# Performance work log

Hardware: AMD Instinct MI355X
Metric: run time of the kernel (lower is better)

The kernel has to match this reference:

```python
import jax, jax.numpy as jnp
import numpy as np

B, C, T = 8, 512, 1024
H = 8
D = C // H          # head_dim = 64
K = 64              # max_rel_dist
REL = 2 * K + 1     # 129


def setup_inputs() -> dict:
    key = jax.random.key(0)
    ks = jax.random.split(key, 12)
    s = 0.02
    return {
        "x": jax.random.normal(ks[0], (B, C, T), jnp.float32),
        "x_mask": jnp.ones((B, 1, T), jnp.float32),
        "W_q": jax.random.normal(ks[1], (C, C), jnp.float32) * s,
        "b_q": jnp.zeros((C,), jnp.float32),
        "W_k": jax.random.normal(ks[2], (C, C), jnp.float32) * s,
        "b_k": jnp.zeros((C,), jnp.float32),
        "W_v": jax.random.normal(ks[3], (C, C), jnp.float32) * s,
        "b_v": jnp.zeros((C,), jnp.float32),
        "W_o": jax.random.normal(ks[4], (C, C), jnp.float32) * s,
        "b_o": jnp.zeros((C,), jnp.float32),
        "emb_rel_k": jax.random.normal(ks[5], (REL, D), jnp.float32) * 0.01,
        "emb_rel_v": jax.random.normal(ks[6], (REL, D), jnp.float32) * 0.01,
    }


def _conv1x1(x, W, b):
    # Conv1d with kernel_size=1: (B,C,T) x (Cout,Cin) -> (B,Cout,T)
    return jnp.einsum("oc,bct->bot", W, x) + b[None, :, None]


def _shape_heads(x):
    # (B,C,T) -> (B,H,T,D)
    b = x.shape[0]
    return x.reshape(b, H, D, T).transpose(0, 1, 3, 2)


def reference(x, x_mask, W_q, b_q, W_k, b_k, W_v, b_v, W_o, b_o, emb_rel_k, emb_rel_v):
    q = _shape_heads(_conv1x1(x, W_q, b_q))  # (B,H,T,D)
    k = _shape_heads(_conv1x1(x, W_k, b_k))
    v = _shape_heads(_conv1x1(x, W_v, b_v))

    # relative position indices: clamp(j - i, -K, K) + K  -> (T,T)
    pos = jnp.arange(T)
    rel_idx = jnp.clip(pos[None, :] - pos[:, None], -K, K) + K

    # scores: scaled QK^T plus unscaled relative-key term (faithful to source)
    attn = jnp.einsum("bhid,bhjd->bhij", q, k) / (D ** 0.5)
    rel_k_tt = emb_rel_k[rel_idx]            # (T,T,D)
    attn = attn + jnp.einsum("bhid,ijd->bhij", q, rel_k_tt)

    # key mask: positions with x_mask <= 0 get -1e9
    key_mask = (x_mask <= 0).reshape(x.shape[0], 1, 1, T)
    attn = jnp.where(key_mask, -1e9, attn)
    attn = jax.nn.softmax(attn, axis=-1)     # dropout p=0.0 -> identity

    y = jnp.einsum("bhij,bhjd->bhid", attn, v)
    rel_v_tt = emb_rel_v[rel_idx]            # (T,T,D)
    y = y + jnp.einsum("bhij,ijd->bhid", attn, rel_v_tt)

    # (B,H,T,D) -> (B,H,D,T) -> (B,C,T)
    y = y.transpose(0, 1, 3, 2).reshape(x.shape[0], C, T)
    y = _conv1x1(y, W_o, b_o)
    return y * x_mask
```

## Files before the change

kernel.cpp:

```cpp
#include <hip/hip_runtime.h>

#define B_   8
#define C_   512
#define T_   1024
#define H_   8
#define D_   64
#define K_   64
#define REL_ 129

typedef unsigned short u16;
typedef __attribute__((ext_vector_type(8))) short short8;
typedef __attribute__((ext_vector_type(4))) float f32x4;

__device__ __forceinline__ float b2f(u16 u) {
    return __uint_as_float(((unsigned)u) << 16);
}
__device__ __forceinline__ u16 f2b(float f) {
    unsigned x = __float_as_uint(f);
    x += 0x7fffu + ((x >> 16) & 1u);
    return (u16)(x >> 16);
}

__global__ __launch_bounds__(256) void cast_all_kernel(
    const float* __restrict__ x,
    const float* __restrict__ Wq, const float* __restrict__ Wk,
    const float* __restrict__ Wv, const float* __restrict__ Wo,
    const float* __restrict__ erk, const float* __restrict__ erv,
    u16* __restrict__ xt, u16* __restrict__ Wh,
    u16* __restrict__ ervt, u16* __restrict__ erkb)
{
    __shared__ u16 tile[64][72];
    const int blk = blockIdx.x;
    const int tid = threadIdx.x;
    if (blk < 1024) {
        const int t0 = (blk & 15) * 64, c0 = ((blk >> 4) & 7) * 64, b = blk >> 7;
        const int f = tid & 15, r0 = tid >> 4;
#pragma unroll
        for (int p = 0; p < 4; ++p) {
            const int c = r0 + p * 16;
            const float4 v = *(const float4*)(x + ((size_t)b * C_ + c0 + c) * T_ + t0 + f * 4);
            tile[c][f * 4 + 0] = f2b(v.x);
            tile[c][f * 4 + 1] = f2b(v.y);
            tile[c][f * 4 + 2] = f2b(v.z);
            tile[c][f * 4 + 3] = f2b(v.w);
        }
        __syncthreads();
#pragma unroll
        for (int p = 0; p < 4; ++p) {
            const int t = r0 + p * 16;
            ushort4 u;
            u.x = tile[f * 4 + 0][t];
            u.y = tile[f * 4 + 1][t];
            u.z = tile[f * 4 + 2][t];
            u.w = tile[f * 4 + 3][t];
            *(ushort4*)(xt + ((size_t)b * T_ + t0 + t) * C_ + c0 + f * 4) = u;
        }
    } else if (blk < 2048) {
        const int gid = (blk - 1024) * 256 + tid;
        const int s = gid >> 16;
        const int off = (gid & 65535) * 4;
        const float* W = (s == 0) ? Wq : (s == 1) ? Wk : (s == 2) ? Wv : Wo;
        const float4 v = *(const float4*)(W + off);
        ushort4 u;
        u.x = f2b(v.x); u.y = f2b(v.y); u.z = f2b(v.z); u.w = f2b(v.w);
        *(ushort4*)(Wh + ((size_t)s << 18) + off) = u;
    } else {
        const int idx = (blk - 2048) * 256 + tid;
        if (idx < 64 * 160) {
            const int d = idx / 160, rel = idx % 160;
            ervt[idx] = (rel < REL_) ? f2b(erv[rel * D_ + d]) : (u16)0;
        } else {
            const int j = idx - 64 * 160;
            if (j < REL_ * D_) erkb[j] = f2b(erk[j]);
        }
    }
}

__global__ __launch_bounds__(256) void proj_mfma(
    const u16* __restrict__ xt, const u16* __restrict__ Wh,
    const float* __restrict__ bq, const float* __restrict__ bk, const float* __restrict__ bv,
    u16* __restrict__ qh, u16* __restrict__ kh, u16* __restrict__ vt)
{
    __shared__ u16 Wt[64][72];

    const int t0 = blockIdx.x * 64;
    const int h  = blockIdx.y;
    const int sel = blockIdx.z >> 3;
    const int b   = blockIdx.z & 7;
    const int tid = threadIdx.x, wave = tid >> 6, lane = tid & 63;
    const int quad = lane >> 4, l16 = lane & 15;

    const u16* Wbase = Wh + ((size_t)sel << 18) + ((size_t)(h * 64) << 9);
    const u16* A = xt + (((size_t)b * T_ + t0 + wave * 16 + l16) << 9);

    const int so = tid >> 2;
    const int sc = (tid & 3) * 16;
    const u16* wsrc = Wbase + ((size_t)so << 9) + sc;

    f32x4 acc[4] = {{0.f,0.f,0.f,0.f},{0.f,0.f,0.f,0.f},{0.f,0.f,0.f,0.f},{0.f,0.f,0.f,0.f}};

    uint4 wv0 = *(const uint4*)(wsrc);
    uint4 wv1 = *(const uint4*)(wsrc + 8);
#pragma unroll 1
    for (int i = 0; i < 8; ++i) {
        const int c0 = i * 64;
        __syncthreads();
        *(uint4*)&Wt[so][sc] = wv0;
        *(uint4*)&Wt[so][sc + 8] = wv1;
        __syncthreads();
        if (i < 7) {
            wv0 = *(const uint4*)(wsrc + c0 + 64);
            wv1 = *(const uint4*)(wsrc + c0 + 72);
        }
#pragma unroll
        for (int kk = 0; kk < 64; kk += 32) {
            const short8 af = *(const short8*)(A + c0 + kk + quad * 8);
#pragma unroll
            for (int nt = 0; nt < 4; ++nt) {
                const short8 bf = *(const short8*)(&Wt[nt * 16 + l16][kk + quad * 8]);
                acc[nt] = __builtin_amdgcn_mfma_f32_16x16x32_bf16(af, bf, acc[nt], 0, 0, 0);
            }
        }
    }

    const float* bias = (sel == 0) ? bq : (sel == 1) ? bk : bv;
    const int bh = b * 8 + h;
#pragma unroll
    for (int nt = 0; nt < 4; ++nt) {
        const int d = nt * 16 + l16;
        const float bo = bias[h * 64 + d];
#pragma unroll
        for (int rix = 0; rix < 4; ++rix) {
            const int t = t0 + wave * 16 + quad * 4 + rix;
            const u16 val = f2b(acc[nt][rix] + bo);
            if (sel == 2) {
                vt[(((size_t)bh * 64 + d) << 10) + t] = val;
            } else {
                u16* dst = sel ? kh : qh;
                dst[(((size_t)bh * T_ + t) << 6) + d] = val;
            }
        }
    }
}

__global__ __launch_bounds__(256, 2) void attn_kernel(
    const u16* __restrict__ qh, const u16* __restrict__ kh, const u16* __restrict__ vt,
    const u16* __restrict__ erkb, const u16* __restrict__ ervt,
    const float* __restrict__ xmask, u16* __restrict__ yf)
{
    __shared__ u16   Sb[32][1032];
    __shared__ u16   sw[32][168];
    __shared__ float red[4][32][2];
    __shared__ float invrow[32];

    const int gid = blockIdx.x;
    const int x8 = gid & 7, r5 = gid >> 3;
    const int bh = x8 + 8 * (r5 >> 5);
    const int i0 = (r5 & 31) * 32;
    const int b = bh >> 3, h = bh & 7;
    const int tid = threadIdx.x, wave = tid >> 6, lane = tid & 63;
    const int quad = lane >> 4, l16 = lane & 15;

    const float LOG2E = 1.4426950408889634f;
    const float SC    = 0.125f * 1.4426950408889634f;

    short8 qa[2][2];
#pragma unroll
    for (int g = 0; g < 2; ++g) {
        const u16* qrow = qh + (((size_t)bh * T_ + i0 + g * 16 + l16) << 6);
        qa[g][0] = *(const short8*)(qrow + quad * 8);
        qa[g][1] = *(const short8*)(qrow + 32 + quad * 8);
    }

    for (int tile = wave; tile < 9; tile += 4) {
        const int rel = tile * 16 + l16;
        const int rl = rel > 128 ? 128 : rel;
        const u16* ep = erkb + rl * 64 + quad * 8;
        const short8 b0 = *(const short8*)(ep);
        const short8 b1 = *(const short8*)(ep + 32);
#pragma unroll
        for (int g = 0; g < 2; ++g) {
            f32x4 m = {0.f, 0.f, 0.f, 0.f};
            m = __builtin_amdgcn_mfma_f32_16x16x32_bf16(qa[g][0], b0, m, 0, 0, 0);
            m = __builtin_amdgcn_mfma_f32_16x16x32_bf16(qa[g][1], b1, m, 0, 0, 0);
            if (rel < 129) {
#pragma unroll
                for (int rix = 0; rix < 4; ++rix)
                    sw[g * 16 + quad * 4 + rix][rel] = f2b(m[rix] * LOG2E);
            }
        }
    }
    __syncthreads();

    float slo_c[2][4], shi_c[2][4];
#pragma unroll
    for (int g = 0; g < 2; ++g)
#pragma unroll
        for (int rix = 0; rix < 4; ++rix) {
            const int row = g * 16 + quad * 4 + rix;
            slo_c[g][rix] = b2f(sw[row][0]);
            shi_c[g][rix] = b2f(sw[row][2 * K_]);
        }

    float psum[2][4] = {{0.f,0.f,0.f,0.f},{0.f,0.f,0.f,0.f}};
    float phi [2][4] = {{0.f,0.f,0.f,0.f},{0.f,0.f,0.f,0.f}};
    f32x4 og[4][2];
#pragma unroll
    for (int s = 0; s < 4; ++s)
#pragma unroll
        for (int g = 0; g < 2; ++g) og[s][g] = (f32x4){0.f, 0.f, 0.f, 0.f};

    {
        const u16* kb = kh + ((size_t)bh << 16);
        const u16* vbase = vt + ((size_t)bh << 16);

        short8 kc0, kc1;
        float  xmc;
        {
            const u16* krow0 = kb + ((size_t)(wave * 256 + l16) << 6);
            kc0 = *(const short8*)(krow0 + quad * 8);
            kc1 = *(const short8*)(krow0 + 32 + quad * 8);
            xmc = xmask[b * T_ + wave * 256 + l16];
        }
        short8 vaf[4];
#pragma unroll
        for (int s = 0; s < 4; ++s)
            vaf[s] = *(const short8*)(vbase + ((size_t)(s * 16 + l16) << 10) + wave * 256 + quad * 8);

#pragma unroll 1
        for (int c = 0; c < 8; ++c) {
#pragma unroll
            for (int half = 0; half < 2; ++half) {
                const int ct = c * 2 + half;
                const int j0 = wave * 256 + ct * 16;
                const int j = j0 + l16;
                const short8 kb0 = kc0, kb1 = kc1;
                const float xmv = xmc;
                {
                    const int jn = wave * 256 + ((ct < 15) ? ct + 1 : ct) * 16 + l16;
                    const u16* krown = kb + ((size_t)jn << 6);
                    kc0 = *(const short8*)(krown + quad * 8);
                    kc1 = *(const short8*)(krown + 32 + quad * 8);
                    xmc = xmask[b * T_ + jn];
                }
                const float clampv = (xmv > 0.f) ? 43.280850f : -2.0e9f;
#pragma unroll
                for (int g = 0; g < 2; ++g) {
                    f32x4 acc = {0.f, 0.f, 0.f, 0.f};
                    acc = __builtin_amdgcn_mfma_f32_16x16x32_bf16(qa[g][0], kb0, acc, 0, 0, 0);
                    acc = __builtin_amdgcn_mfma_f32_16x16x32_bf16(qa[g][1], kb1, acc, 0, 0, 0);
                    const int dd = j0 - (i0 + g * 16);
                    const int ibase = i0 + g * 16 + quad * 4;
                    float ee[4];
                    if (dd <= -79) {
#pragma unroll
                        for (int rix = 0; rix < 4; ++rix)
                            ee[rix] = __builtin_amdgcn_exp2f(
                                fminf(fmaf(acc[rix], SC, slo_c[g][rix]), clampv));
                    } else if (dd >= 79) {
#pragma unroll
                        for (int rix = 0; rix < 4; ++rix)
                            ee[rix] = __builtin_amdgcn_exp2f(
                                fminf(fmaf(acc[rix], SC, shi_c[g][rix]), clampv));
                    } else {
                        const int relb = j - ibase + K_;
#pragma unroll
                        for (int rix = 0; rix < 4; ++rix) {
                            int idx = relb - rix;
                            idx = idx < 0 ? 0 : (idx > 2 * K_ ? 2 * K_ : idx);
                            const int row = g * 16 + quad * 4 + rix;
                            const float sr = b2f(sw[row][idx]);
                            ee[rix] = __builtin_amdgcn_exp2f(
                                fminf(fmaf(acc[rix], SC, sr), clampv));
                        }
                    }
                    unsigned p01, p23;
                    asm("v_cvt_pk_bf16_f32 %0, %1, %2" : "=v"(p01) : "v"(ee[0]), "v"(ee[1]));
                    asm("v_cvt_pk_bf16_f32 %0, %1, %2" : "=v"(p23) : "v"(ee[2]), "v"(ee[3]));
                    const int r0 = g * 16 + quad * 4;
                    Sb[r0 + 0][j] = (u16)(p01 & 0xffffu);
                    Sb[r0 + 1][j] = (u16)(p01 >> 16);
                    Sb[r0 + 2][j] = (u16)(p23 & 0xffffu);
                    Sb[r0 + 3][j] = (u16)(p23 >> 16);
                    const float er0 = __uint_as_float(p01 << 16);
                    const float er1 = __uint_as_float(p01 & 0xffff0000u);
                    const float er2 = __uint_as_float(p23 << 16);
                    const float er3 = __uint_as_float(p23 & 0xffff0000u);
                    psum[g][0] += er0; psum[g][1] += er1;
                    psum[g][2] += er2; psum[g][3] += er3;
                    if (dd >= 79) {
                        phi[g][0] += er0; phi[g][1] += er1;
                        phi[g][2] += er2; phi[g][3] += er3;
                    } else if (dd > -79) {
                        phi[g][0] += (j - ibase >= 64) ? er0 : 0.f;
                        phi[g][1] += (j - ibase >= 65) ? er1 : 0.f;
                        phi[g][2] += (j - ibase >= 66) ? er2 : 0.f;
                        phi[g][3] += (j - ibase >= 67) ? er3 : 0.f;
                    }
                }
            }
            const int kc = wave * 256 + c * 32;
            const short8 pb0 = *(const short8*)(&Sb[l16][kc + quad * 8]);
            const short8 pb1 = *(const short8*)(&Sb[16 + l16][kc + quad * 8]);
            short8 vn[4];
            {
                const int kcn = wave * 256 + ((c < 7) ? c + 1 : c) * 32;
#pragma unroll
                for (int s = 0; s < 4; ++s)
                    vn[s] = *(const short8*)(vbase + ((size_t)(s * 16 + l16) << 10) + kcn + quad * 8);
            }
#pragma unroll
            for (int s = 0; s < 4; ++s) {
                og[s][0] = __builtin_amdgcn_mfma_f32_16x16x32_bf16(vaf[s], pb0, og[s][0], 0, 0, 0);
                og[s][1] = __builtin_amdgcn_mfma_f32_16x16x32_bf16(vaf[s], pb1, og[s][1], 0, 0, 0);
            }
#pragma unroll
            for (int s = 0; s < 4; ++s) vaf[s] = vn[s];
        }
#pragma unroll
        for (int m = 1; m < 16; m <<= 1)
#pragma unroll
            for (int g = 0; g < 2; ++g)
#pragma unroll
                for (int rix = 0; rix < 4; ++rix) {
                    psum[g][rix] += __shfl_xor(psum[g][rix], m);
                    phi[g][rix]  += __shfl_xor(phi[g][rix], m);
                }
        if (l16 == 0)
#pragma unroll
            for (int g = 0; g < 2; ++g)
#pragma unroll
                for (int rix = 0; rix < 4; ++rix) {
                    const int row = g * 16 + quad * 4 + rix;
                    red[wave][row][0] = psum[g][rix];
                    red[wave][row][1] = phi[g][rix];
                }
    }
    __syncthreads();

    {
        const int rr = tid >> 3;
        const int c0 = tid & 7;
        const float sumrow = red[0][rr][0] + red[1][rr][0] + red[2][rr][0] + red[3][rr][0];
        const float phirow = red[0][rr][1] + red[1][rr][1] + red[2][rr][1] + red[3][rr][1];
        float intsum = 0.f;
        for (int rel = c0; rel < 168; rel += 8) {
            if (rel == 0 || rel == 2 * K_) continue;
            u16 v = 0;
            if (rel < 2 * K_) {
                const int j = i0 + rr + rel - K_;
                if (j >= 0 && j < T_) v = Sb[rr][j];
                intsum += b2f(v);
            }
            sw[rr][rel] = v;
        }
        intsum += __shfl_xor(intsum, 1);
        intsum += __shfl_xor(intsum, 2);
        intsum += __shfl_xor(intsum, 4);
        if (c0 == 0) {
            sw[rr][2 * K_] = f2b(phirow);
            sw[rr][0]      = f2b(sumrow - intsum - phirow);
            invrow[rr]     = 1.0f / sumrow;
        }
    }
    __syncthreads();

    float* fog = (float*)&Sb[0][0];
#pragma unroll
    for (int s = 0; s < 4; ++s)
#pragma unroll
        for (int g = 0; g < 2; ++g)
            *(f32x4*)&fog[wave * 2048 + ((s * 2 + g) * 64 + lane) * 4] = og[s][g];
    __syncthreads();

    {
        const int dh = wave * 16 + l16;
        const u16* ep = ervt + dh * 160;
        f32x4 accg[2];
#pragma unroll
        for (int g = 0; g < 2; ++g) {
            const int base = ((wave * 2 + g) * 64 + lane) * 4;
            f32x4 a0 = *(const f32x4*)&fog[base];
            f32x4 a1 = *(const f32x4*)&fog[2048 + base];
            f32x4 a2 = *(const f32x4*)&fog[4096 + base];
            f32x4 a3 = *(const f32x4*)&fog[6144 + base];
#pragma unroll
            for (int rix = 0; rix < 4; ++rix)
                accg[g][rix] = (a0[rix] + a1[rix]) + (a2[rix] + a3[rix]);
        }
#pragma unroll
        for (int kt = 0; kt < 5; ++kt) {
            const short8 af = *(const short8*)(ep + kt * 32 + quad * 8);
            const short8 p0 = *(const short8*)(&sw[l16][kt * 32 + quad * 8]);
            const short8 p1 = *(const short8*)(&sw[16 + l16][kt * 32 + quad * 8]);
            accg[0] = __builtin_amdgcn_mfma_f32_16x16x32_bf16(af, p0, accg[0], 0, 0, 0);
            accg[1] = __builtin_amdgcn_mfma_f32_16x16x32_bf16(af, p1, accg[1], 0, 0, 0);
        }
        const int dbase = (h << 6) + wave * 16 + quad * 4;
#pragma unroll
        for (int g = 0; g < 2; ++g) {
            const float iv = invrow[g * 16 + l16];
            ushort4 u;
            u.x = f2b(accg[g][0] * iv); u.y = f2b(accg[g][1] * iv);
            u.z = f2b(accg[g][2] * iv); u.w = f2b(accg[g][3] * iv);
            *(ushort4*)(yf + (((size_t)b * T_ + i0 + g * 16 + l16) << 9) + dbase) = u;
        }
    }
}

__global__ __launch_bounds__(256) void outproj_mfma(
    const u16* __restrict__ yf, const u16* __restrict__ Woh, const float* __restrict__ bo,
    const float* __restrict__ xmask, float* __restrict__ out)
{
    __shared__ u16 Yt[64][72];

    const int o0 = blockIdx.x * 64;
    const int b  = blockIdx.y >> 4;
    const int t0 = (blockIdx.y & 15) * 64;
    const int tid = threadIdx.x, wave = tid >> 6, lane = tid & 63;
    const int quad = lane >> 4, l16 = lane & 15;

    const u16* A = Woh + ((size_t)(o0 + wave * 16 + l16) << 9);

    const int so = tid >> 2;
    const int sc = (tid & 3) * 16;
    const u16* ysrc = yf + (((size_t)b * T_ + t0 + so) << 9) + sc;

    f32x4 acc[4] = {{0.f,0.f,0.f,0.f},{0.f,0.f,0.f,0.f},{0.f,0.f,0.f,0.f},{0.f,0.f,0.f,0.f}};

    uint4 wv0 = *(const uint4*)(ysrc);
    uint4 wv1 = *(const uint4*)(ysrc + 8);
#pragma unroll 1
    for (int i = 0; i < 8; ++i) {
        const int c0 = i * 64;
        __syncthreads();
        *(uint4*)&Yt[so][sc] = wv0;
        *(uint4*)&Yt[so][sc + 8] = wv1;
        __syncthreads();
        if (i < 7) {
            wv0 = *(const uint4*)(ysrc + c0 + 64);
            wv1 = *(const uint4*)(ysrc + c0 + 72);
        }
#pragma unroll
        for (int kk = 0; kk < 64; kk += 32) {
            const short8 af = *(const short8*)(A + c0 + kk + quad * 8);
#pragma unroll
            for (int nt = 0; nt < 4; ++nt) {
                const short8 bf = *(const short8*)(&Yt[nt * 16 + l16][kk + quad * 8]);
                acc[nt] = __builtin_amdgcn_mfma_f32_16x16x32_bf16(af, bf, acc[nt], 0, 0, 0);
            }
        }
    }

#pragma unroll
    for (int nt = 0; nt < 4; ++nt) {
        const int t = t0 + nt * 16 + l16;
        const float xmv = xmask[b * T_ + t];
#pragma unroll
        for (int rix = 0; rix < 4; ++rix) {
            const int o = o0 + wave * 16 + quad * 4 + rix;
            out[((size_t)b * C_ + o) * T_ + t] = (acc[nt][rix] + bo[o]) * xmv;
        }
    }
}

extern "C" void kernel_launch(void* const* d_in, const int* in_sizes, int n_in,
                              void* d_out, int out_size, void* d_ws, size_t ws_size,
                              hipStream_t stream) {
    const float* x     = (const float*)d_in[0];
    const float* xmask = (const float*)d_in[1];
    const float* Wq    = (const float*)d_in[2];
    const float* bq    = (const float*)d_in[3];
    const float* Wk    = (const float*)d_in[4];
    const float* bk    = (const float*)d_in[5];
    const float* Wv    = (const float*)d_in[6];
    const float* bv    = (const float*)d_in[7];
    const float* Wo    = (const float*)d_in[8];
    const float* bo    = (const float*)d_in[9];
    const float* erk   = (const float*)d_in[10];
    const float* erv   = (const float*)d_in[11];

    const size_t need = 44077184;
    if (ws_size < need) return;
    u16* xt   = (u16*)d_ws;
    u16* Wh   = (u16*)((char*)d_ws + 8388608);
    u16* qh   = (u16*)((char*)d_ws + 10485760);
    u16* kh   = (u16*)((char*)d_ws + 18874368);
    u16* vt   = (u16*)((char*)d_ws + 27262976);
    u16* yf   = (u16*)((char*)d_ws + 35651584);
    u16* ervt = (u16*)((char*)d_ws + 44040192);
    u16* erkb = (u16*)((char*)d_ws + 44060672);
    float* out = (float*)d_out;

    cast_all_kernel<<<dim3(2121), 256, 0, stream>>>(
        x, Wq, Wk, Wv, Wo, erk, erv, xt, Wh, ervt, erkb);
    proj_mfma<<<dim3(T_ / 64, H_, 3 * B_), 256, 0, stream>>>(
        xt, Wh, bq, bk, bv, qh, kh, vt);
    attn_kernel<<<dim3(2048), 256, 0, stream>>>(
        qh, kh, vt, erkb, ervt, xmask, yf);
    outproj_mfma<<<dim3(C_ / 64, B_ * (T_ / 64)), 256, 0, stream>>>(
        yf, Wh + ((size_t)3 << 18), bo, xmask, out);
}
```

Before: 232.0 us.

## Fuse Q/K/V projections into one block and stage V transpose through shared memory

The projection kernel now computes Q, K and V for the same token tile in a single block, so each A fragment of x is loaded once and reused across all three weight matrices, and the grid shrinks threefold. The V output is first written to a shared-memory tile and then stored to the transposed vt layout with 16-byte coalesced writes, replacing scattered 2-byte strided stores. The cost is three times the accumulator registers and more LDS per block, which may lower occupancy, and there are fewer blocks to spread across the GPU.

```diff
diff --git a/kernel.cpp b/kernel.cpp
--- a/kernel.cpp
+++ b/kernel.cpp
@@ -81,65 +81,97 @@
     const float* __restrict__ bq, const float* __restrict__ bk, const float* __restrict__ bv,
     u16* __restrict__ qh, u16* __restrict__ kh, u16* __restrict__ vt)
 {
-    __shared__ u16 Wt[64][72];
+    __shared__ u16 Wt[3][64][72];
+    __shared__ u16 vtile[64][72];
 
     const int t0 = blockIdx.x * 64;
     const int h  = blockIdx.y;
-    const int sel = blockIdx.z >> 3;
-    const int b   = blockIdx.z & 7;
+    const int b  = blockIdx.z;
     const int tid = threadIdx.x, wave = tid >> 6, lane = tid & 63;
     const int quad = lane >> 4, l16 = lane & 15;
 
-    const u16* Wbase = Wh + ((size_t)sel << 18) + ((size_t)(h * 64) << 9);
     const u16* A = xt + (((size_t)b * T_ + t0 + wave * 16 + l16) << 9);
 
     const int so = tid >> 2;
     const int sc = (tid & 3) * 16;
-    const u16* wsrc = Wbase + ((size_t)so << 9) + sc;
-
-    f32x4 acc[4] = {{0.f,0.f,0.f,0.f},{0.f,0.f,0.f,0.f},{0.f,0.f,0.f,0.f},{0.f,0.f,0.f,0.f}};
-
-    uint4 wv0 = *(const uint4*)(wsrc);
-    uint4 wv1 = *(const uint4*)(wsrc + 8);
+    const u16* wsrc0 = Wh + ((size_t)0 << 18) + ((size_t)(h * 64 + so) << 9) + sc;
+    const u16* wsrc1 = Wh + ((size_t)1 << 18) + ((size_t)(h * 64 + so) << 9) + sc;
+    const u16* wsrc2 = Wh + ((size_t)2 << 18) + ((size_t)(h * 64 + so) << 9) + sc;
+
+    f32x4 acc[3][4];
+#pragma unroll
+    for (int s = 0; s < 3; ++s)
+#pragma unroll
+        for (int nt = 0; nt < 4; ++nt) acc[s][nt] = (f32x4){0.f, 0.f, 0.f, 0.f};
+
+    uint4 wv[3][2];
+    wv[0][0] = *(const uint4*)(wsrc0); wv[0][1] = *(const uint4*)(wsrc0 + 8);
+    wv[1][0] = *(const uint4*)(wsrc1); wv[1][1] = *(const uint4*)(wsrc1 + 8);
+    wv[2][0] = *(const uint4*)(wsrc2); wv[2][1] = *(const uint4*)(wsrc2 + 8);
+
 #pragma unroll 1
     for (int i = 0; i < 8; ++i) {
         const int c0 = i * 64;
         __syncthreads();
-        *(uint4*)&Wt[so][sc] = wv0;
-        *(uint4*)&Wt[so][sc + 8] = wv1;
+#pragma unroll
+        for (int s = 0; s < 3; ++s) {
+            *(uint4*)&Wt[s][so][sc] = wv[s][0];
+            *(uint4*)&Wt[s][so][sc + 8] = wv[s][1];
+        }
         __syncthreads();
         if (i < 7) {
-            wv0 = *(const uint4*)(wsrc + c0 + 64);
-            wv1 = *(const uint4*)(wsrc + c0 + 72);
+            wv[0][0] = *(const uint4*)(wsrc0 + c0 + 64); wv[0][1] = *(const uint4*)(wsrc0 + c0 + 72);
+            wv[1][0] = *(const uint4*)(wsrc1 + c0 + 64); wv[1][1] = *(const uint4*)(wsrc1 + c0 + 72);
+            wv[2][0] = *(const uint4*)(wsrc2 + c0 + 64); wv[2][1] = *(const uint4*)(wsrc2 + c0 + 72);
         }
 #pragma unroll
         for (int kk = 0; kk < 64; kk += 32) {
             const short8 af = *(const short8*)(A + c0 + kk + quad * 8);
 #pragma unroll
-            for (int nt = 0; nt < 4; ++nt) {
-                const short8 bf = *(const short8*)(&Wt[nt * 16 + l16][kk + quad * 8]);
-                acc[nt] = __builtin_amdgcn_mfma_f32_16x16x32_bf16(af, bf, acc[nt], 0, 0, 0);
-            }
-        }
-    }
-
-    const float* bias = (sel == 0) ? bq : (sel == 1) ? bk : bv;
+            for (int s = 0; s < 3; ++s)
+#pragma unroll
+                for (int nt = 0; nt < 4; ++nt) {
+                    const short8 bf = *(const short8*)(&Wt[s][nt * 16 + l16][kk + quad * 8]);
+                    acc[s][nt] = __builtin_amdgcn_mfma_f32_16x16x32_bf16(af, bf, acc[s][nt], 0, 0, 0);
+                }
+        }
+    }
+
     const int bh = b * 8 + h;
+#pragma unroll
+    for (int s = 0; s < 2; ++s) {
+        const float* bias = s ? bk : bq;
+        u16* dst = s ? kh : qh;
+#pragma unroll
+        for (int nt = 0; nt < 4; ++nt) {
+            const int d = nt * 16 + l16;
+            const float bo = bias[h * 64 + d];
+#pragma unroll
+            for (int rix = 0; rix < 4; ++rix) {
+                const int t = t0 + wave * 16 + quad * 4 + rix;
+                dst[(((size_t)bh * T_ + t) << 6) + d] = f2b(acc[s][nt][rix] + bo);
+            }
+        }
+    }
 #pragma unroll
     for (int nt = 0; nt < 4; ++nt) {
         const int d = nt * 16 + l16;
-        const float bo = bias[h * 64 + d];
+        const float bo = bv[h * 64 + d];
 #pragma unroll
         for (int rix = 0; rix < 4; ++rix) {
-            const int t = t0 + wave * 16 + quad * 4 + rix;
-            const u16 val = f2b(acc[nt][rix] + bo);
-            if (sel == 2) {
-                vt[(((size_t)bh * 64 + d) << 10) + t] = val;
-            } else {
-                u16* dst = sel ? kh : qh;
-                dst[(((size_t)bh * T_ + t) << 6) + d] = val;
-            }
-        }
+            const int tl = wave * 16 + quad * 4 + rix;
+            vtile[d][tl] = f2b(acc[2][nt][rix] + bo);
+        }
+    }
+    __syncthreads();
+    {
+        const int row = tid >> 2;
+        const int seg = (tid & 3) * 16;
+        const uint4 v0 = *(const uint4*)&vtile[row][seg];
+        const uint4 v1 = *(const uint4*)&vtile[row][seg + 8];
+        u16* vdst = vt + (((size_t)bh * 64 + row) << 10) + t0 + seg;
+        *(uint4*)(vdst) = v0;
+        *(uint4*)(vdst + 8) = v1;
     }
 }
 
@@ -494,7 +526,7 @@
 
     cast_all_kernel<<<dim3(2121), 256, 0, stream>>>(
         x, Wq, Wk, Wv, Wo, erk, erv, xt, Wh, ervt, erkb);
-    proj_mfma<<<dim3(T_ / 64, H_, 3 * B_), 256, 0, stream>>>(
+    proj_mfma<<<dim3(T_ / 64, H_, B_), 256, 0, stream>>>(
         xt, Wh, bq, bk, bv, qh, kh, vt);
     attn_kernel<<<dim3(2048), 256, 0, stream>>>(
         qh, kh, vt, erkb, ervt, xmask, yf);
```

Result: slower. 281.4 us (+21.3%).
